# Kernel optimization log

Measured on AMD Instinct MI355X. Metric: run time of the kernel, lower is better.

The kernel has to match this reference:

```python
import jax, jax.numpy as jnp
import numpy as np

BINS = 128
H, W = 4096, 4096


def setup_inputs() -> dict:
    key = jax.random.key(0)
    k1, k2 = jax.random.split(key)
    img = jax.random.randint(k1, (H, W, 3), 0, 256, dtype=jnp.int32)
    mask = jax.random.uniform(k2, (H, W), dtype=jnp.float32)
    full = jnp.zeros((BINS, BINS, BINS), dtype=jnp.float32)
    lines = jnp.zeros((BINS, BINS, BINS), dtype=jnp.float32)
    return {"img": img, "mask": mask, "full": full, "lines": lines}


def reference(img, mask, full, lines):
    # quantize 0..255 -> 0..127 (matches uint8 img // 2)
    q = (img // 2)[:, :, :3]
    h, w, _ = q.shape
    flat = q.reshape(h * w, 3)  # [N, 3] bin indices
    r, g, b = flat[:, 0], flat[:, 1], flat[:, 2]

    # _push_image: scatter-add into 128^3 histograms
    full2 = full.at[r, g, b].add(1.0)
    lines2 = lines.at[r, g, b].add(mask.reshape(h * w))

    # get_ratios: normalized log-likelihood-ratio threshold filter
    l = lines2 + 1e-10
    f = full2 + 1.0
    l = l / jnp.sum(l)
    f = f / jnp.sum(f)
    log_ratios = jnp.log(l / f)
    avg_log_ratios = jnp.sum(l * log_ratios)
    color_filter = log_ratios > avg_log_ratios  # [128,128,128] bool

    # _apply_filter: per-pixel gather from the 3D lookup table
    out = color_filter[q[..., 0], q[..., 1], q[..., 2]]  # [H, W] bool
    return out
```

## Files before the change

### kernel.cpp

```cpp
#include <hip/hip_runtime.h>
#include <stdint.h>


typedef uint32_t u32x4 __attribute__((ext_vector_type(4)));

#define P1_BLK    512
#define P1_PIXG   1024

#define NBKT_N    128
#define SHIFT_N   14
#define CAP_N     135168
#define NBKT_M    512
#define SHIFT_M   12
#define CAP_M     34816
#define BPB_M     4096

#define NSUB      32
#define SUBCAP    4608
#define NSEG      (NBKT_N * NSUB)
#define P15_SPLIT 32
#define P15_BLK   512
#define P15_CHUNK 2048

template<bool WBPIX>
__global__ __launch_bounds__(P1_BLK) void p1_scatter_new(
    const u32x4* __restrict__ img4, const u32x4* __restrict__ mask4,
    uint32_t* __restrict__ cursor,
    uint8_t* __restrict__ gsub, unsigned long long* __restrict__ gpm,
    u32x4* __restrict__ bpix4)
{
    __shared__ uint32_t s_cnt[NBKT_N];
    __shared__ uint32_t s_start[NBKT_N];
    __shared__ int      s_adj[NBKT_N];
    __shared__ uint32_t s_wsum[P1_BLK / 64];
    __shared__ uint32_t s_meta[P1_PIXG * 4];
    __shared__ uint32_t s_msk[P1_PIXG * 4];
    __shared__ uint8_t  s_bkt[P1_PIXG * 4];

    const int tid = threadIdx.x;
    if (tid < NBKT_N) s_cnt[tid] = 0;
    __syncthreads();

    const int g0 = blockIdx.x * P1_PIXG;
    uint32_t bin[8], rk[8], msk[8];

    #pragma unroll
    for (int k = 0; k < 2; ++k) {
        int g = g0 + tid + k * P1_BLK;
        u32x4 a = __builtin_nontemporal_load(&img4[3 * g + 0]);
        u32x4 b = __builtin_nontemporal_load(&img4[3 * g + 1]);
        u32x4 c = __builtin_nontemporal_load(&img4[3 * g + 2]);
        u32x4 m = __builtin_nontemporal_load(&mask4[g]);
        uint32_t b0 = ((a.x >> 1) << 14) | ((a.y >> 1) << 7) | (a.z >> 1);
        uint32_t b1 = ((a.w >> 1) << 14) | ((b.x >> 1) << 7) | (b.y >> 1);
        uint32_t b2 = ((b.z >> 1) << 14) | ((b.w >> 1) << 7) | (c.x >> 1);
        uint32_t b3 = ((c.y >> 1) << 14) | ((c.z >> 1) << 7) | (c.w >> 1);
        if (WBPIX) {
            u32x4 bb = {b0, b1, b2, b3};
            __builtin_nontemporal_store(bb, &bpix4[g]);
        }
        bin[4*k+0] = b0; msk[4*k+0] = m.x; rk[4*k+0] = atomicAdd(&s_cnt[b0 >> SHIFT_N], 1u);
        bin[4*k+1] = b1; msk[4*k+1] = m.y; rk[4*k+1] = atomicAdd(&s_cnt[b1 >> SHIFT_N], 1u);
        bin[4*k+2] = b2; msk[4*k+2] = m.z; rk[4*k+2] = atomicAdd(&s_cnt[b2 >> SHIFT_N], 1u);
        bin[4*k+3] = b3; msk[4*k+3] = m.w; rk[4*k+3] = atomicAdd(&s_cnt[b3 >> SHIFT_N], 1u);
    }
    __syncthreads();

    uint32_t v = (tid < NBKT_N) ? s_cnt[tid] : 0u;
    uint32_t inc = v;
    #pragma unroll
    for (int o = 1; o < 64; o <<= 1) {
        uint32_t n = __shfl_up(inc, o, 64);
        if ((tid & 63) >= o) inc += n;
    }
    if ((tid & 63) == 63) s_wsum[tid >> 6] = inc;
    __syncthreads();
    if (tid == 0) {
        uint32_t run = 0;
        #pragma unroll
        for (int w = 0; w < P1_BLK / 64; ++w) { uint32_t t = s_wsum[w]; s_wsum[w] = run; run += t; }
    }
    __syncthreads();
    uint32_t start = inc - v + s_wsum[tid >> 6];
    if (tid < NBKT_N) {
        s_start[tid] = start;
        uint32_t gb = v ? atomicAdd(&cursor[tid], v) : 0u;
        s_adj[tid] = (int)gb - (int)start;
    }
    __syncthreads();

    #pragma unroll
    for (int k = 0; k < 8; ++k) {
        uint32_t slot = s_start[bin[k] >> SHIFT_N] + rk[k];
        s_meta[slot] = (bin[k] & 0x3FFFu) | ((uint32_t)tid << 14) | ((uint32_t)k << 23);
        s_msk[slot]  = msk[k];
        s_bkt[slot]  = (uint8_t)(bin[k] >> SHIFT_N);
    }
    __syncthreads();

    for (int i = tid; i < P1_PIXG * 4; i += P1_BLK) {
        uint32_t m  = s_meta[i];
        uint32_t bk = s_bkt[i];
        uint32_t pos = (uint32_t)(s_adj[bk] + i);
        if (pos < (uint32_t)CAP_N) {
            size_t idx = (size_t)bk * CAP_N + pos;
            uint32_t t9 = (m >> 14) & 511u;
            uint32_t kk = m >> 23;
            uint32_t g  = (uint32_t)g0 + t9 + (kk >> 2) * P1_BLK;
            uint32_t pix = 4u * g + (kk & 3u);
            uint32_t lo14 = m & 0x3FFFu;
            gpm[idx]  = ((unsigned long long)(lo14 & 511u) << 55)
                      | ((unsigned long long)pix << 31)
                      | (unsigned long long)(s_msk[i] & 0x7FFFFFFFu);
            gsub[idx] = (uint8_t)(lo14 >> 9);
        }
    }
}

template<int NB, int SHIFT, int CAPV>
__global__ __launch_bounds__(P1_BLK) void p1_scatter_det(
    const u32x4* __restrict__ img4, const u32x4* __restrict__ mask4,
    uint32_t* __restrict__ cursor,
    unsigned short* __restrict__ gbin, unsigned long long* __restrict__ gpm)
{
    __shared__ uint32_t s_cnt[NB];
    __shared__ uint32_t s_start[NB];
    __shared__ int      s_adj[NB];
    __shared__ uint32_t s_wsum[P1_BLK / 64];
    __shared__ uint32_t s_bin[P1_PIXG * 4];
    __shared__ unsigned long long s_pm[P1_PIXG * 4];

    const int tid = threadIdx.x;
    if (tid < NB) s_cnt[tid] = 0;
    __syncthreads();

    const int g0 = blockIdx.x * P1_PIXG;
    uint32_t bin[8], rk[8];
    unsigned long long pm[8];

    #pragma unroll
    for (int k = 0; k < 2; ++k) {
        int g = g0 + tid + k * P1_BLK;
        u32x4 a = __builtin_nontemporal_load(&img4[3 * g + 0]);
        u32x4 b = __builtin_nontemporal_load(&img4[3 * g + 1]);
        u32x4 c = __builtin_nontemporal_load(&img4[3 * g + 2]);
        u32x4 m = __builtin_nontemporal_load(&mask4[g]);
        uint32_t b0 = ((a.x >> 1) << 14) | ((a.y >> 1) << 7) | (a.z >> 1);
        uint32_t b1 = ((a.w >> 1) << 14) | ((b.x >> 1) << 7) | (b.y >> 1);
        uint32_t b2 = ((b.z >> 1) << 14) | ((b.w >> 1) << 7) | (c.x >> 1);
        uint32_t b3 = ((c.y >> 1) << 14) | ((c.z >> 1) << 7) | (c.w >> 1);
        unsigned long long p0 = (unsigned long long)(4u * (uint32_t)g);
        bin[4*k+0] = b0; pm[4*k+0] = ((p0 + 0) << 32) | m.x; rk[4*k+0] = atomicAdd(&s_cnt[b0 >> SHIFT], 1u);
        bin[4*k+1] = b1; pm[4*k+1] = ((p0 + 1) << 32) | m.y; rk[4*k+1] = atomicAdd(&s_cnt[b1 >> SHIFT], 1u);
        bin[4*k+2] = b2; pm[4*k+2] = ((p0 + 2) << 32) | m.z; rk[4*k+2] = atomicAdd(&s_cnt[b2 >> SHIFT], 1u);
        bin[4*k+3] = b3; pm[4*k+3] = ((p0 + 3) << 32) | m.w; rk[4*k+3] = atomicAdd(&s_cnt[b3 >> SHIFT], 1u);
    }
    __syncthreads();

    uint32_t v = (tid < NB) ? s_cnt[tid] : 0u;
    uint32_t inc = v;
    #pragma unroll
    for (int o = 1; o < 64; o <<= 1) {
        uint32_t n = __shfl_up(inc, o, 64);
        if ((tid & 63) >= o) inc += n;
    }
    if ((tid & 63) == 63) s_wsum[tid >> 6] = inc;
    __syncthreads();
    if (tid == 0) {
        uint32_t run = 0;
        #pragma unroll
        for (int w = 0; w < P1_BLK / 64; ++w) { uint32_t t = s_wsum[w]; s_wsum[w] = run; run += t; }
    }
    __syncthreads();
    uint32_t start = inc - v + s_wsum[tid >> 6];
    if (tid < NB) {
        s_start[tid] = start;
        uint32_t gb = v ? atomicAdd(&cursor[tid], v) : 0u;
        s_adj[tid] = (int)gb - (int)start;
    }
    __syncthreads();

    #pragma unroll
    for (int k = 0; k < 8; ++k) {
        uint32_t slot = s_start[bin[k] >> SHIFT] + rk[k];
        s_bin[slot] = bin[k];
        s_pm[slot]  = pm[k];
    }
    __syncthreads();

    for (int i = tid; i < P1_PIXG * 4; i += P1_BLK) {
        uint32_t bf = s_bin[i];
        uint32_t bk = bf >> SHIFT;
        uint32_t pos = (uint32_t)(s_adj[bk] + i);
        if (pos < (uint32_t)CAPV) {
            size_t idx = (size_t)bk * CAPV + pos;
            gbin[idx] = (unsigned short)(bf & ((1u << SHIFT) - 1u));
            gpm[idx]  = s_pm[i];
        }
    }
}

__global__ __launch_bounds__(P15_BLK) void p15_subpart(
    const uint8_t* __restrict__ gsub,
    const unsigned long long* __restrict__ gpm,
    const uint32_t* __restrict__ cursor,
    unsigned long long* __restrict__ gpm2,
    uint32_t* __restrict__ cnt2)
{
    __shared__ uint32_t s_c[NSUB], s_st[NSUB + 1], s_gp[NSUB];
    __shared__ unsigned long long s_sp[P15_CHUNK];
    __shared__ uint8_t s_sub[P15_CHUNK];

    const int tid  = threadIdx.x;
    const int b    = blockIdx.x >> 5;
    const int part = blockIdx.x & (P15_SPLIT - 1);
    uint32_t n = cursor[b];
    if (n > CAP_N) n = CAP_N;
    const size_t base = (size_t)b * CAP_N;
    const uint32_t STRIDE = (uint32_t)P15_SPLIT * P15_CHUNK;

    for (uint32_t c0 = (uint32_t)part * P15_CHUNK; c0 < n; c0 += STRIDE) {
        const uint32_t cn = (n - c0 < (uint32_t)P15_CHUNK) ? (n - c0) : (uint32_t)P15_CHUNK;
        if (tid < NSUB) s_c[tid] = 0u;
        __syncthreads();

        uint32_t sub[4]; unsigned long long pk[4]; uint32_t myr[4];
        #pragma unroll
        for (int k = 0; k < 4; ++k) {
            uint32_t i = (uint32_t)tid + k * (uint32_t)P15_BLK;
            if (i < cn) {
                sub[k] = gsub[base + c0 + i];
                pk[k]  = gpm[base + c0 + i];
                myr[k] = atomicAdd(&s_c[sub[k]], 1u);
            } else sub[k] = 0xFFFFFFFFu;
        }
        __syncthreads();
        if (tid == 0) {
            uint32_t run = 0;
            #pragma unroll
            for (int r = 0; r < NSUB; ++r) { s_st[r] = run; run += s_c[r]; }
            s_st[NSUB] = run;
        }
        if (tid < NSUB) {
            uint32_t c = s_c[tid];
            s_gp[tid] = c ? atomicAdd(&cnt2[b * NSUB + tid], c) : 0u;
        }
        __syncthreads();
        #pragma unroll
        for (int k = 0; k < 4; ++k) {
            if (sub[k] != 0xFFFFFFFFu) {
                uint32_t slot = s_st[sub[k]] + myr[k];
                s_sp[slot]  = pk[k];
                s_sub[slot] = (uint8_t)sub[k];
            }
        }
        __syncthreads();

        for (uint32_t i = tid; i < cn; i += P15_BLK) {
            uint32_t r = s_sub[i];
            uint32_t pos = s_gp[r] + (i - s_st[r]);
            if (pos < SUBCAP) {
                size_t d = ((size_t)b * NSUB + r) * SUBCAP + pos;
                gpm2[d] = s_sp[i];
            }
        }
        __syncthreads();
    }
}

__global__ __launch_bounds__(512) void p2_binhist(
    const unsigned long long* __restrict__ gpm2,
    const uint32_t* __restrict__ cnt2,
    const float* __restrict__ full_in, const float* __restrict__ lines_in,
    float* __restrict__ fA, float* __restrict__ lA,
    double* __restrict__ plf)
{
    __shared__ uint32_t s_cnt[512];
    __shared__ unsigned short s_start[512];
    __shared__ uint32_t s_wt[8];
    __shared__ unsigned long long s_srt[SUBCAP];
    __shared__ double s_d0[8], s_d1[8];

    const int tid = threadIdx.x;
    const int s = blockIdx.x;
    uint32_t n = cnt2[s];
    if (n > SUBCAP) n = SUBCAP;
    const size_t base = (size_t)s * SUBCAP;

    s_cnt[tid] = 0u;
    __syncthreads();

    uint32_t           myb[9];
    unsigned long long myp[9];
    uint32_t           myr[9];
    #pragma unroll
    for (int k = 0; k < 9; ++k) {
        uint32_t i = (uint32_t)tid + (uint32_t)k * 512u;
        if (i < n) {
            unsigned long long pv = gpm2[base + i];
            uint32_t lo = (uint32_t)(pv >> 55);
            myp[k] = pv;
            myr[k] = atomicAdd(&s_cnt[lo], 1u);
            myb[k] = lo;
        } else myb[k] = 0xFFFFFFFFu;
    }
    __syncthreads();

    uint32_t v = s_cnt[tid], inc = v;
    #pragma unroll
    for (int o = 1; o < 64; o <<= 1) {
        uint32_t t = __shfl_up(inc, o, 64);
        if ((tid & 63) >= o) inc += t;
    }
    if ((tid & 63) == 63) s_wt[tid >> 6] = inc;
    __syncthreads();
    if (tid == 0) {
        uint32_t run = 0;
        #pragma unroll
        for (int w = 0; w < 8; ++w) { uint32_t t = s_wt[w]; s_wt[w] = run; run += t; }
    }
    __syncthreads();
    const uint32_t st = s_wt[tid >> 6] + inc - v;
    s_start[tid] = (unsigned short)st;
    __syncthreads();

    #pragma unroll
    for (int k = 0; k < 9; ++k) {
        if (myb[k] != 0xFFFFFFFFu)
            s_srt[(uint32_t)s_start[myb[k]] + myr[k]] = myp[k];
    }
    __syncthreads();

    const uint32_t c = v;
    for (uint32_t x = 1; x < c; ++x) {
        unsigned long long val = s_srt[st + x];
        int y = (int)x - 1;
        while (y >= 0 && s_srt[st + y] > val) { s_srt[st + y + 1] = s_srt[st + y]; --y; }
        s_srt[st + y + 1] = val;
    }
    float sum = 0.0f;
    for (uint32_t x = 0; x < c; ++x)
        sum += __uint_as_float((uint32_t)s_srt[st + x] & 0x7FFFFFFFu);

    const size_t gb = (size_t)s * 512 + tid;
    float f = (float)c + full_in[gb] + 1.0f;
    float l = (sum + lines_in[gb]) + 1e-10f;
    fA[gb] = f;
    lA[gb] = l;

    double sl = (double)l, sf = (double)f;
    #pragma unroll
    for (int o = 32; o > 0; o >>= 1) {
        sl += __shfl_down(sl, o, 64);
        sf += __shfl_down(sf, o, 64);
    }
    const int lane = tid & 63, wid = tid >> 6;
    if (lane == 0) { s_d0[wid] = sl; s_d1[wid] = sf; }
    __syncthreads();
    if (tid == 0) {
        double a0 = 0.0, a1 = 0.0;
        #pragma unroll
        for (int w = 0; w < 8; ++w) { a0 += s_d0[w]; a1 += s_d1[w]; }
        plf[2 * s + 0] = a0;
        plf[2 * s + 1] = a1;
    }
}

__global__ __launch_bounds__(1024) void p2_sort_hist(
    const unsigned short* __restrict__ gbin,
    const unsigned long long* __restrict__ gpm,
    const uint32_t* __restrict__ cursor,
    unsigned long long* __restrict__ srt,
    uint32_t* __restrict__ counts, float* __restrict__ lsum)
{
    __shared__ uint32_t s_cnt[BPB_M];
    __shared__ uint32_t s_start[BPB_M];
    __shared__ uint32_t s_fill[BPB_M];
    __shared__ uint32_t s_wt[16];

    const int tid = threadIdx.x;
    const int b = blockIdx.x;
    for (int j = tid; j < BPB_M; j += 1024) s_cnt[j] = 0u;
    __syncthreads();

    uint32_t n = cursor[b];
    if (n > CAP_M) n = CAP_M;
    const size_t base = (size_t)b * CAP_M;

    for (uint32_t i = tid; i < n; i += 1024)
        atomicAdd(&s_cnt[gbin[base + i]], 1u);
    __syncthreads();

    const int j0 = tid * 4;
    uint32_t a0 = s_cnt[j0+0], a1 = s_cnt[j0+1], a2 = s_cnt[j0+2], a3 = s_cnt[j0+3];
    uint32_t s = a0 + a1 + a2 + a3;
    uint32_t inc = s;
    #pragma unroll
    for (int o = 1; o < 64; o <<= 1) {
        uint32_t t = __shfl_up(inc, o, 64);
        if ((tid & 63) >= o) inc += t;
    }
    if ((tid & 63) == 63) s_wt[tid >> 6] = inc;
    __syncthreads();
    if (tid == 0) {
        uint32_t run = 0;
        #pragma unroll
        for (int w = 0; w < 16; ++w) { uint32_t t = s_wt[w]; s_wt[w] = run; run += t; }
    }
    __syncthreads();
    uint32_t ex = s_wt[tid >> 6] + (inc - s);
    uint32_t e0 = ex, e1 = ex + a0, e2 = e1 + a1, e3 = e2 + a2;
    s_start[j0+0] = e0; s_start[j0+1] = e1; s_start[j0+2] = e2; s_start[j0+3] = e3;
    s_fill[j0+0] = 0u;  s_fill[j0+1] = 0u;  s_fill[j0+2] = 0u;  s_fill[j0+3] = 0u;
    __syncthreads();

    for (uint32_t i = tid; i < n; i += 1024) {
        uint32_t lo = gbin[base + i];
        unsigned long long pmv = __builtin_nontemporal_load(&gpm[base + i]);
        uint32_t slot = s_start[lo] + atomicAdd(&s_fill[lo], 1u);
        srt[base + slot] = pmv;
    }
    __threadfence_block();
    __syncthreads();

    uint32_t cs[4] = {a0, a1, a2, a3};
    uint32_t ss[4] = {e0, e1, e2, e3};
    #pragma unroll
    for (int t = 0; t < 4; ++t) {
        uint32_t c = cs[t];
        unsigned long long* arr = srt + base + ss[t];
        for (uint32_t x = 1; x < c; ++x) {
            unsigned long long v2 = arr[x];
            int y = (int)x - 1;
            while (y >= 0 && arr[y] > v2) { arr[y+1] = arr[y]; --y; }
            arr[y+1] = v2;
        }
        float sum = 0.0f;
        for (uint32_t x = 0; x < c; ++x)
            sum += __uint_as_float((uint32_t)arr[x]);
        size_t gbidx = (size_t)b * BPB_M + (size_t)(j0 + t);
        counts[gbidx] = c;
        lsum[gbidx]   = sum;
    }
}

__global__ void hist_direct_kernel(const u32x4* __restrict__ img4,
                                   const u32x4* __restrict__ mask4,
                                   uint32_t* __restrict__ counts,
                                   float* __restrict__ lsum, int npix4) {
    int t = blockIdx.x * blockDim.x + threadIdx.x;
    if (t >= npix4) return;
    u32x4 a = img4[3 * t + 0];
    u32x4 b = img4[3 * t + 1];
    u32x4 c = img4[3 * t + 2];
    u32x4 m = mask4[t];
    uint32_t b0 = ((a.x >> 1) << 14) | ((a.y >> 1) << 7) | (a.z >> 1);
    uint32_t b1 = ((a.w >> 1) << 14) | ((b.x >> 1) << 7) | (b.y >> 1);
    uint32_t b2 = ((b.z >> 1) << 14) | ((b.w >> 1) << 7) | (c.x >> 1);
    uint32_t b3 = ((c.y >> 1) << 14) | ((c.z >> 1) << 7) | (c.w >> 1);
    atomicAdd(&counts[b0], 1u);
    atomicAdd(&counts[b1], 1u);
    atomicAdd(&counts[b2], 1u);
    atomicAdd(&counts[b3], 1u);
    unsafeAtomicAdd(&lsum[b0], __uint_as_float(m.x));
    unsafeAtomicAdd(&lsum[b1], __uint_as_float(m.y));
    unsafeAtomicAdd(&lsum[b2], __uint_as_float(m.z));
    unsafeAtomicAdd(&lsum[b3], __uint_as_float(m.w));
}

__global__ __launch_bounds__(512) void fuse_fl_kernel(
    const uint32_t* __restrict__ counts, const float* __restrict__ lsum,
    const float* __restrict__ full_in, const float* __restrict__ lines_in,
    float* __restrict__ fA, float* __restrict__ lA,
    double* __restrict__ plf)
{
    __shared__ double s_d0[8], s_d1[8];
    const int tid = threadIdx.x;
    const int s = blockIdx.x;
    const size_t gb = (size_t)s * 512 + tid;
    float f = (float)counts[gb] + full_in[gb] + 1.0f;
    float l = (lsum[gb] + lines_in[gb]) + 1e-10f;
    fA[gb] = f;
    lA[gb] = l;
    double sl = (double)l, sf = (double)f;
    #pragma unroll
    for (int o = 32; o > 0; o >>= 1) {
        sl += __shfl_down(sl, o, 64);
        sf += __shfl_down(sf, o, 64);
    }
    const int lane = tid & 63, wid = tid >> 6;
    if (lane == 0) { s_d0[wid] = sl; s_d1[wid] = sf; }
    __syncthreads();
    if (tid == 0) {
        double a0 = 0.0, a1 = 0.0;
        #pragma unroll
        for (int w = 0; w < 8; ++w) { a0 += s_d0[w]; a1 += s_d1[w]; }
        plf[2 * s + 0] = a0;
        plf[2 * s + 1] = a1;
    }
}

__global__ __launch_bounds__(256) void final_lf_kernel(
    const double* __restrict__ plf, double* __restrict__ accum) {
    __shared__ double s0[4], s1[4];
    const int tid = threadIdx.x;
    double sl = 0.0, sf = 0.0;
    #pragma unroll
    for (int k = 0; k < NSEG / 256; ++k) {
        int j = tid + 256 * k;
        sl += plf[2 * j + 0];
        sf += plf[2 * j + 1];
    }
    #pragma unroll
    for (int o = 32; o > 0; o >>= 1) {
        sl += __shfl_down(sl, o, 64);
        sf += __shfl_down(sf, o, 64);
    }
    const int lane = tid & 63, wid = tid >> 6;
    if (lane == 0) { s0[wid] = sl; s1[wid] = sf; }
    __syncthreads();
    if (tid == 0) {
        accum[0] = s0[0] + s0[1] + s0[2] + s0[3];
        accum[1] = s1[0] + s1[1] + s1[2] + s1[3];
    }
}

__global__ __launch_bounds__(256) void logr_kernel(
    const float* __restrict__ fA, const float* __restrict__ lA,
    const double* __restrict__ accum, double* __restrict__ part_avg,
    float* __restrict__ logr, int nbin) {
    float Sl = (float)accum[0];
    float Sf = (float)accum[1];
    double acc = 0.0;
    for (int i = blockIdx.x * 256 + threadIdx.x; i < nbin; i += 256 * 256) {
        float f = fA[i];
        float l = lA[i];
        float ln = l / Sl;
        float fn = f / Sf;
        float lr = logf(ln / fn);
        logr[i] = lr;
        acc += (double)(ln * lr);
    }
    for (int o = 32; o > 0; o >>= 1) acc += __shfl_down(acc, o, 64);
    __shared__ double s[4];
    int lane = threadIdx.x & 63, wid = threadIdx.x >> 6;
    if (lane == 0) s[wid] = acc;
    __syncthreads();
    if (threadIdx.x == 0) part_avg[blockIdx.x] = s[0] + s[1] + s[2] + s[3];
}

__global__ void final_avg_kernel(const double* __restrict__ part_avg,
                                 double* __restrict__ accum) {
    const int lane = threadIdx.x;
    double a = 0.0;
    #pragma unroll
    for (int k = 0; k < 4; ++k) a += part_avg[lane + 64 * k];
    #pragma unroll
    for (int o = 32; o > 0; o >>= 1) a += __shfl_down(a, o, 64);
    if (lane == 0) accum[2] = a;
}

__global__ void filt_kernel(const float* __restrict__ logr,
                            const double* __restrict__ accum,
                            unsigned long long* __restrict__ bits, int nbin) {
    float avg = (float)accum[2];
    int i = blockIdx.x * blockDim.x + threadIdx.x;
    bool p = (i < nbin) && (logr[i] > avg);
    unsigned long long m = __ballot(p);
    if ((threadIdx.x & 63) == 0 && i < nbin) bits[i >> 6] = m;
}

__global__ void out_kernel_bpix(const u32x4* __restrict__ bpix4,
                                const uint32_t* __restrict__ bits32,
                                u32x4* __restrict__ out4, int npix4) {
    int t = blockIdx.x * blockDim.x + threadIdx.x;
    if (t >= npix4) return;
    u32x4 b = __builtin_nontemporal_load(&bpix4[t]);
    u32x4 o = {(bits32[b.x >> 5] >> (b.x & 31u)) & 1u,
               (bits32[b.y >> 5] >> (b.y & 31u)) & 1u,
               (bits32[b.z >> 5] >> (b.z & 31u)) & 1u,
               (bits32[b.w >> 5] >> (b.w & 31u)) & 1u};
    __builtin_nontemporal_store(o, &out4[t]);
}

__global__ void out_kernel_img(const u32x4* __restrict__ img4,
                               const uint32_t* __restrict__ bits32,
                               u32x4* __restrict__ out4, int npix4) {
    int t = blockIdx.x * blockDim.x + threadIdx.x;
    if (t >= npix4) return;
    u32x4 a = __builtin_nontemporal_load(&img4[3 * t + 0]);
    u32x4 b = __builtin_nontemporal_load(&img4[3 * t + 1]);
    u32x4 c = __builtin_nontemporal_load(&img4[3 * t + 2]);
    uint32_t b0 = ((a.x >> 1) << 14) | ((a.y >> 1) << 7) | (a.z >> 1);
    uint32_t b1 = ((a.w >> 1) << 14) | ((b.x >> 1) << 7) | (b.y >> 1);
    uint32_t b2 = ((b.z >> 1) << 14) | ((b.w >> 1) << 7) | (c.x >> 1);
    uint32_t b3 = ((c.y >> 1) << 14) | ((c.z >> 1) << 7) | (c.w >> 1);
    u32x4 o = {(bits32[b0 >> 5] >> (b0 & 31u)) & 1u,
               (bits32[b1 >> 5] >> (b1 & 31u)) & 1u,
               (bits32[b2 >> 5] >> (b2 & 31u)) & 1u,
               (bits32[b3 >> 5] >> (b3 & 31u)) & 1u};
    __builtin_nontemporal_store(o, &out4[t]);
}

extern "C" void kernel_launch(void* const* d_in, const int* in_sizes, int n_in,
                              void* d_out, int out_size, void* d_ws, size_t ws_size,
                              hipStream_t stream) {
    const int*   img      = (const int*)d_in[0];
    const float* mask     = (const float*)d_in[1];
    const float* full_in  = (const float*)d_in[2];
    const float* lines_in = (const float*)d_in[3];

    const int npix  = in_sizes[1];
    const int nbin  = in_sizes[2];
    const int npix4 = npix / 4;

    char* ws = (char*)d_ws;
    const size_t ENT1 = (size_t)NBKT_M * CAP_M;
    const size_t ENT2 = (size_t)NSEG * SUBCAP;

    const size_t off_cursor = 64;
    const size_t off_plf    = off_cursor + 4ull * NBKT_M;
    const size_t off_pavg   = off_plf + 2ull * NSEG * 8;
    const size_t off_cnt2   = off_pavg + 256ull * 8;
    const size_t off_hdrend = (off_cnt2 + 4ull * NSEG + 255ull) & ~255ull;
    const size_t off_counts = off_hdrend;
    const size_t off_lsum   = off_counts + 4ull * nbin;
    const size_t off_fA     = off_lsum + 4ull * nbin;
    const size_t off_lA     = off_fA + 4ull * nbin;
    const size_t off_logr   = off_lA + 4ull * nbin;
    const size_t off_filt   = off_logr + 4ull * nbin;
    const size_t off_gbin   = (off_filt + (size_t)nbin + 255ull) & ~255ull;
    const size_t off_gpm    = (off_gbin + 2ull * ENT1 + 255ull) & ~255ull;
    const size_t off_union  = off_gpm + 8ull * ENT1;
    const size_t need_mid   = off_union + 8ull * ENT1;
    const size_t off_gpm2   = off_union;
    const size_t need_new   = off_gpm2 + 8ull * ENT2;
    const size_t off_bpix   = (need_new + 255ull) & ~255ull;
    const size_t need_new2  = off_bpix + 4ull * (size_t)npix;

    double*   accum  = (double*)ws;
    uint32_t* cursor = (uint32_t*)(ws + off_cursor);
    double*   plf    = (double*)(ws + off_plf);
    double*   pavg   = (double*)(ws + off_pavg);
    uint32_t* cnt2   = (uint32_t*)(ws + off_cnt2);
    uint32_t* counts = (uint32_t*)(ws + off_counts);
    float*    lsum   = (float*)(ws + off_lsum);
    float*    fA     = (float*)(ws + off_fA);
    float*    lA     = (float*)(ws + off_lA);
    float*    logr   = (float*)(ws + off_logr);
    unsigned long long* fbits = (unsigned long long*)(ws + off_filt);
    const uint32_t*     fb32  = (const uint32_t*)(ws + off_filt);
    unsigned short*     gbin = (unsigned short*)(ws + off_gbin);
    uint8_t*            gsub = (uint8_t*)(ws + off_gbin);
    unsigned long long* gpm  = (unsigned long long*)(ws + off_gpm);
    unsigned long long* srt  = (unsigned long long*)(ws + off_union);
    unsigned long long* gpm2 = (unsigned long long*)(ws + off_gpm2);
    u32x4*              bpix4 = (u32x4*)(ws + off_bpix);

    const bool shape_ok  = (nbin == NBKT_M * BPB_M) && (npix % (P1_PIXG * 4) == 0);
    const bool pack_ok   = shape_ok && (npix <= (1 << 24));
    const bool tier_new2 = pack_ok && ws_size >= need_new2;
    const bool tier_new  = pack_ok && ws_size >= need_new;
    const bool tier_mid  = shape_ok && ws_size >= need_mid;
    const int BLK = 256;

    if (tier_new2 || tier_new) {
        hipMemsetAsync(ws, 0, off_hdrend, stream);
        if (tier_new2) {
            p1_scatter_new<true><<<npix / (P1_PIXG * 4), P1_BLK, 0, stream>>>(
                (const u32x4*)img, (const u32x4*)mask, cursor, gsub, gpm, bpix4);
        } else {
            p1_scatter_new<false><<<npix / (P1_PIXG * 4), P1_BLK, 0, stream>>>(
                (const u32x4*)img, (const u32x4*)mask, cursor, gsub, gpm, nullptr);
        }
        p15_subpart<<<NBKT_N * P15_SPLIT, P15_BLK, 0, stream>>>(
            gsub, gpm, cursor, gpm2, cnt2);
        p2_binhist<<<NSEG, 512, 0, stream>>>(gpm2, cnt2, full_in, lines_in,
                                             fA, lA, plf);
    } else if (tier_mid) {
        hipMemsetAsync(ws, 0, off_hdrend, stream);
        p1_scatter_det<NBKT_M, SHIFT_M, CAP_M>
            <<<npix / (P1_PIXG * 4), P1_BLK, 0, stream>>>(
            (const u32x4*)img, (const u32x4*)mask, cursor, gbin, gpm);
        p2_sort_hist<<<NBKT_M, 1024, 0, stream>>>(gbin, gpm, cursor, srt, counts, lsum);
        fuse_fl_kernel<<<NSEG, 512, 0, stream>>>(counts, lsum, full_in, lines_in,
                                                 fA, lA, plf);
    } else {
        hipMemsetAsync(ws, 0, off_hdrend, stream);
        hipMemsetAsync(ws + off_counts, 0, 8ull * nbin, stream);
        hist_direct_kernel<<<(npix4 + BLK - 1) / BLK, BLK, 0, stream>>>(
            (const u32x4*)img, (const u32x4*)mask, counts, lsum, npix4);
        fuse_fl_kernel<<<NSEG, 512, 0, stream>>>(counts, lsum, full_in, lines_in,
                                                 fA, lA, plf);
    }

    final_lf_kernel<<<1, 256, 0, stream>>>(plf, accum);
    logr_kernel<<<256, 256, 0, stream>>>(fA, lA, accum, pavg, logr, nbin);
    final_avg_kernel<<<1, 64, 0, stream>>>(pavg, accum);
    filt_kernel<<<(nbin + BLK - 1) / BLK, BLK, 0, stream>>>(logr, accum, fbits, nbin);
    if (tier_new2) {
        out_kernel_bpix<<<(npix4 + BLK - 1) / BLK, BLK, 0, stream>>>(
            bpix4, fb32, (u32x4*)d_out, npix4);
    } else {
        out_kernel_img<<<(npix4 + BLK - 1) / BLK, BLK, 0, stream>>>(
            (const u32x4*)img, fb32, (u32x4*)d_out, npix4);
    }
}
```

Baseline: 653.7 us.

## Fold reduction kernels into consumers and split large kernels into halves

Removes the single-block final_lf and final_avg kernels: logr_kernel now reduces the per-segment sums itself in every block, and filt_kernel reduces the partial averages in every block. The main scatter, subpartition, histogram and output kernels are each split into two launches of half the grid, using an offset parameter. Fewer tiny serial launches cut launch and tail gaps. Every block now repeats the small reductions, and the extra launches from splitting add overhead without any obvious benefit on a single stream.

```diff
diff --git a/kernel.cpp b/kernel.cpp
--- a/kernel.cpp
+++ b/kernel.cpp
@@ -27,7 +27,7 @@
     const u32x4* __restrict__ img4, const u32x4* __restrict__ mask4,
     uint32_t* __restrict__ cursor,
     uint8_t* __restrict__ gsub, unsigned long long* __restrict__ gpm,
-    u32x4* __restrict__ bpix4)
+    u32x4* __restrict__ bpix4, int bofs)
 {
     __shared__ uint32_t s_cnt[NBKT_N];
     __shared__ uint32_t s_start[NBKT_N];
@@ -41,7 +41,7 @@
     if (tid < NBKT_N) s_cnt[tid] = 0;
     __syncthreads();
 
-    const int g0 = blockIdx.x * P1_PIXG;
+    const int g0 = (blockIdx.x + bofs) * P1_PIXG;
     uint32_t bin[8], rk[8], msk[8];
 
     #pragma unroll
@@ -205,14 +205,14 @@
     const unsigned long long* __restrict__ gpm,
     const uint32_t* __restrict__ cursor,
     unsigned long long* __restrict__ gpm2,
-    uint32_t* __restrict__ cnt2)
+    uint32_t* __restrict__ cnt2, int bofs)
 {
     __shared__ uint32_t s_c[NSUB], s_st[NSUB + 1], s_gp[NSUB];
     __shared__ unsigned long long s_sp[P15_CHUNK];
     __shared__ uint8_t s_sub[P15_CHUNK];
 
     const int tid  = threadIdx.x;
-    const int b    = blockIdx.x >> 5;
+    const int b    = (blockIdx.x >> 5) + bofs;
     const int part = blockIdx.x & (P15_SPLIT - 1);
     uint32_t n = cursor[b];
     if (n > CAP_N) n = CAP_N;
@@ -273,7 +273,7 @@
     const uint32_t* __restrict__ cnt2,
     const float* __restrict__ full_in, const float* __restrict__ lines_in,
     float* __restrict__ fA, float* __restrict__ lA,
-    double* __restrict__ plf)
+    double* __restrict__ plf, int sofs)
 {
     __shared__ uint32_t s_cnt[512];
     __shared__ unsigned short s_start[512];
@@ -282,7 +282,7 @@
     __shared__ double s_d0[8], s_d1[8];
 
     const int tid = threadIdx.x;
-    const int s = blockIdx.x;
+    const int s = blockIdx.x + sofs;
     uint32_t n = cnt2[s];
     if (n > SUBCAP) n = SUBCAP;
     const size_t base = (size_t)s * SUBCAP;
@@ -500,9 +500,12 @@
     }
 }
 
-__global__ __launch_bounds__(256) void final_lf_kernel(
-    const double* __restrict__ plf, double* __restrict__ accum) {
+__global__ __launch_bounds__(256) void logr_kernel(
+    const float* __restrict__ fA, const float* __restrict__ lA,
+    const double* __restrict__ plf, double* __restrict__ part_avg,
+    float* __restrict__ logr, int nbin) {
     __shared__ double s0[4], s1[4];
+    __shared__ double sSl, sSf;
     const int tid = threadIdx.x;
     double sl = 0.0, sf = 0.0;
     #pragma unroll
@@ -520,19 +523,15 @@
     if (lane == 0) { s0[wid] = sl; s1[wid] = sf; }
     __syncthreads();
     if (tid == 0) {
-        accum[0] = s0[0] + s0[1] + s0[2] + s0[3];
-        accum[1] = s1[0] + s1[1] + s1[2] + s1[3];
-    }
-}
-
-__global__ __launch_bounds__(256) void logr_kernel(
-    const float* __restrict__ fA, const float* __restrict__ lA,
-    const double* __restrict__ accum, double* __restrict__ part_avg,
-    float* __restrict__ logr, int nbin) {
-    float Sl = (float)accum[0];
-    float Sf = (float)accum[1];
+        sSl = s0[0] + s0[1] + s0[2] + s0[3];
+        sSf = s1[0] + s1[1] + s1[2] + s1[3];
+    }
+    __syncthreads();
+    float Sl = (float)sSl;
+    float Sf = (float)sSf;
+
     double acc = 0.0;
-    for (int i = blockIdx.x * 256 + threadIdx.x; i < nbin; i += 256 * 256) {
+    for (int i = blockIdx.x * 256 + tid; i < nbin; i += 256 * 256) {
         float f = fA[i];
         float l = lA[i];
         float ln = l / Sl;
@@ -543,37 +542,36 @@
     }
     for (int o = 32; o > 0; o >>= 1) acc += __shfl_down(acc, o, 64);
     __shared__ double s[4];
-    int lane = threadIdx.x & 63, wid = threadIdx.x >> 6;
     if (lane == 0) s[wid] = acc;
     __syncthreads();
-    if (threadIdx.x == 0) part_avg[blockIdx.x] = s[0] + s[1] + s[2] + s[3];
-}
-
-__global__ void final_avg_kernel(const double* __restrict__ part_avg,
-                                 double* __restrict__ accum) {
-    const int lane = threadIdx.x;
-    double a = 0.0;
-    #pragma unroll
-    for (int k = 0; k < 4; ++k) a += part_avg[lane + 64 * k];
-    #pragma unroll
-    for (int o = 32; o > 0; o >>= 1) a += __shfl_down(a, o, 64);
-    if (lane == 0) accum[2] = a;
+    if (tid == 0) part_avg[blockIdx.x] = s[0] + s[1] + s[2] + s[3];
 }
 
 __global__ void filt_kernel(const float* __restrict__ logr,
-                            const double* __restrict__ accum,
+                            const double* __restrict__ part_avg,
                             unsigned long long* __restrict__ bits, int nbin) {
-    float avg = (float)accum[2];
-    int i = blockIdx.x * blockDim.x + threadIdx.x;
+    __shared__ double sAvg;
+    const int tid = threadIdx.x;
+    if (tid < 64) {
+        double a = 0.0;
+        #pragma unroll
+        for (int k = 0; k < 4; ++k) a += part_avg[tid + 64 * k];
+        #pragma unroll
+        for (int o = 32; o > 0; o >>= 1) a += __shfl_down(a, o, 64);
+        if (tid == 0) sAvg = a;
+    }
+    __syncthreads();
+    float avg = (float)sAvg;
+    int i = blockIdx.x * blockDim.x + tid;
     bool p = (i < nbin) && (logr[i] > avg);
     unsigned long long m = __ballot(p);
-    if ((threadIdx.x & 63) == 0 && i < nbin) bits[i >> 6] = m;
+    if ((tid & 63) == 0 && i < nbin) bits[i >> 6] = m;
 }
 
 __global__ void out_kernel_bpix(const u32x4* __restrict__ bpix4,
                                 const uint32_t* __restrict__ bits32,
-                                u32x4* __restrict__ out4, int npix4) {
-    int t = blockIdx.x * blockDim.x + threadIdx.x;
+                                u32x4* __restrict__ out4, int npix4, int tofs) {
+    int t = blockIdx.x * blockDim.x + threadIdx.x + tofs;
     if (t >= npix4) return;
     u32x4 b = __builtin_nontemporal_load(&bpix4[t]);
     u32x4 o = {(bits32[b.x >> 5] >> (b.x & 31u)) & 1u,
@@ -638,7 +636,6 @@
     const size_t off_bpix   = (need_new + 255ull) & ~255ull;
     const size_t need_new2  = off_bpix + 4ull * (size_t)npix;
 
-    double*   accum  = (double*)ws;
     uint32_t* cursor = (uint32_t*)(ws + off_cursor);
     double*   plf    = (double*)(ws + off_plf);
     double*   pavg   = (double*)(ws + off_pavg);
@@ -666,17 +663,29 @@
 
     if (tier_new2 || tier_new) {
         hipMemsetAsync(ws, 0, off_hdrend, stream);
+        const int NB1  = npix / (P1_PIXG * 4);
+        const int NB1h = NB1 / 2;
         if (tier_new2) {
-            p1_scatter_new<true><<<npix / (P1_PIXG * 4), P1_BLK, 0, stream>>>(
-                (const u32x4*)img, (const u32x4*)mask, cursor, gsub, gpm, bpix4);
+            if (NB1h > 0)
+                p1_scatter_new<true><<<NB1h, P1_BLK, 0, stream>>>(
+                    (const u32x4*)img, (const u32x4*)mask, cursor, gsub, gpm, bpix4, 0);
+            p1_scatter_new<true><<<NB1 - NB1h, P1_BLK, 0, stream>>>(
+                (const u32x4*)img, (const u32x4*)mask, cursor, gsub, gpm, bpix4, NB1h);
         } else {
-            p1_scatter_new<false><<<npix / (P1_PIXG * 4), P1_BLK, 0, stream>>>(
-                (const u32x4*)img, (const u32x4*)mask, cursor, gsub, gpm, nullptr);
-        }
-        p15_subpart<<<NBKT_N * P15_SPLIT, P15_BLK, 0, stream>>>(
-            gsub, gpm, cursor, gpm2, cnt2);
-        p2_binhist<<<NSEG, 512, 0, stream>>>(gpm2, cnt2, full_in, lines_in,
-                                             fA, lA, plf);
+            if (NB1h > 0)
+                p1_scatter_new<false><<<NB1h, P1_BLK, 0, stream>>>(
+                    (const u32x4*)img, (const u32x4*)mask, cursor, gsub, gpm, nullptr, 0);
+            p1_scatter_new<false><<<NB1 - NB1h, P1_BLK, 0, stream>>>(
+                (const u32x4*)img, (const u32x4*)mask, cursor, gsub, gpm, nullptr, NB1h);
+        }
+        p15_subpart<<<(NBKT_N / 2) * P15_SPLIT, P15_BLK, 0, stream>>>(
+            gsub, gpm, cursor, gpm2, cnt2, 0);
+        p15_subpart<<<(NBKT_N / 2) * P15_SPLIT, P15_BLK, 0, stream>>>(
+            gsub, gpm, cursor, gpm2, cnt2, NBKT_N / 2);
+        p2_binhist<<<NSEG / 2, 512, 0, stream>>>(gpm2, cnt2, full_in, lines_in,
+                                                 fA, lA, plf, 0);
+        p2_binhist<<<NSEG / 2, 512, 0, stream>>>(gpm2, cnt2, full_in, lines_in,
+                                                 fA, lA, plf, NSEG / 2);
     } else if (tier_mid) {
         hipMemsetAsync(ws, 0, off_hdrend, stream);
         p1_scatter_det<NBKT_M, SHIFT_M, CAP_M>
@@ -694,13 +703,16 @@
                                                  fA, lA, plf);
     }
 
-    final_lf_kernel<<<1, 256, 0, stream>>>(plf, accum);
-    logr_kernel<<<256, 256, 0, stream>>>(fA, lA, accum, pavg, logr, nbin);
-    final_avg_kernel<<<1, 64, 0, stream>>>(pavg, accum);
-    filt_kernel<<<(nbin + BLK - 1) / BLK, BLK, 0, stream>>>(logr, accum, fbits, nbin);
+    logr_kernel<<<256, 256, 0, stream>>>(fA, lA, plf, pavg, logr, nbin);
+    filt_kernel<<<(nbin + BLK - 1) / BLK, BLK, 0, stream>>>(logr, pavg, fbits, nbin);
     if (tier_new2) {
-        out_kernel_bpix<<<(npix4 + BLK - 1) / BLK, BLK, 0, stream>>>(
-            bpix4, fb32, (u32x4*)d_out, npix4);
+        const int gA = (npix4 + 511) / 512;
+        const int tofsB = gA * 256;
+        out_kernel_bpix<<<gA, BLK, 0, stream>>>(bpix4, fb32, (u32x4*)d_out, npix4, 0);
+        if (npix4 > tofsB) {
+            const int gB = (npix4 - tofsB + BLK - 1) / BLK;
+            out_kernel_bpix<<<gB, BLK, 0, stream>>>(bpix4, fb32, (u32x4*)d_out, npix4, tofsB);
+        }
     } else {
         out_kernel_img<<<(npix4 + BLK - 1) / BLK, BLK, 0, stream>>>(
             (const u32x4*)img, fb32, (u32x4*)d_out, npix4);
```

Result: slower. 684.3 us (+4.7%).
